# Kernel tuning notes

Hardware: AMD Instinct MI355X
Metric: run time of the kernel (lower is better)

The kernel has to match this reference:

```python
import jax, jax.numpy as jnp
import numpy as np

N_NODES = 50000
N_EDGES = 800000
IN_C, HID_C, OUT_C = 128, 256, 128


def _gcn_conv(x, src, dst, W, b, num_nodes):
    # PyG GCNConv: self-loops + symmetric normalization + linear + scatter-add
    deg = jax.ops.segment_sum(jnp.ones_like(src, x.dtype), dst, num_segments=num_nodes)
    dinv = jnp.where(deg > 0, jax.lax.rsqrt(deg), 0.0)
    norm = dinv[src] * dinv[dst]                      # [E']
    h = x @ W.T                                       # [N, C_out] transform first (C_out usually < C_in path cost)
    msg = h[src] * norm[:, None]                      # [E', C_out] gather + scale
    out = jax.ops.segment_sum(msg, dst, num_segments=num_nodes)  # scatter-add
    return out + b


def setup_inputs() -> dict:
    key = jax.random.key(0)
    k1, k2, k3, k4 = jax.random.split(key, 4)
    x = jax.random.normal(k1, (N_NODES, IN_C), dtype=jnp.float32)
    edge_index = jax.random.randint(k2, (2, N_EDGES), 0, N_NODES, dtype=jnp.int64)
    W1 = jax.random.normal(k3, (HID_C, IN_C), dtype=jnp.float32) * (1.0 / np.sqrt(IN_C))
    b1 = jnp.zeros((HID_C,), dtype=jnp.float32)
    W2 = jax.random.normal(k4, (OUT_C, HID_C), dtype=jnp.float32) * (1.0 / np.sqrt(HID_C))
    b2 = jnp.zeros((OUT_C,), dtype=jnp.float32)
    return {"x": x, "edge_index": edge_index, "W1": W1, "b1": b1,
            "W2": W2, "b2": b2, "num_nodes": N_NODES}


def reference(x, edge_index, W1, b1, W2, b2, num_nodes):
    # add self-loops once (shared by both layers)
    loop = jnp.arange(num_nodes, dtype=edge_index.dtype)
    src = jnp.concatenate([edge_index[0], loop])
    dst = jnp.concatenate([edge_index[1], loop])
    h = _gcn_conv(x, src, dst, W1, b1, num_nodes)
    h = jax.nn.relu(h)
    out = _gcn_conv(h, src, dst, W2, b2, num_nodes)
    return out
```

## Files before the change

kernel.cpp:

```cpp
#include <hip/hip_runtime.h>

#define N_NODES 50000
#define N_EDGES 800000
#define IN_C 128
#define HID_C 256
#define OUT_C 128
#define NBLK 196
#define NPART 8
#define PART_W 6250
#define KB2 32
#define CHUNK (N_EDGES / KB2)
#define HW_HIST 256
#define HW_W 16
#define SC_SCAT 256
#define SC_XC 1563

typedef __attribute__((ext_vector_type(8))) short short8v;
typedef __attribute__((ext_vector_type(4))) float f32x4;

static __device__ __forceinline__ unsigned short f2bf(float f) {
  unsigned int u = __float_as_uint(f);
  unsigned int r = (u + 0x7fffu + ((u >> 16) & 1u)) >> 16;
  return (unsigned short)r;
}
static __device__ __forceinline__ float bf2f(unsigned short h) {
  return __uint_as_float(((unsigned int)h) << 16);
}
static __device__ __forceinline__ unsigned int packBF2(float a, float b) {
  return (unsigned int)f2bf(a) | ((unsigned int)f2bf(b) << 16);
}

static __device__ __forceinline__ int detect64(const int* __restrict__ ei) {
  int nz = 0;
#pragma unroll
  for (int k = 0; k < 64; ++k) nz |= ei[2 * k + 1];
  return (nz == 0) ? 1 : 0;
}
static __device__ __forceinline__ int load_dst(const int* __restrict__ ei,
                                               int is64, int e) {
  return is64 ? (int)((const uint2*)ei)[N_EDGES + e].x : ei[N_EDGES + e];
}
static __device__ __forceinline__ int load_src(const int* __restrict__ ei,
                                               int is64, int e) {
  return is64 ? (int)((const uint2*)ei)[e].x : ei[e];
}

__global__ __launch_bounds__(1024) void hist_wconv_k(const int* __restrict__ ei,
                                                     int* __restrict__ H,
                                                     const float* __restrict__ W1,
                                                     unsigned int* __restrict__ w1bf,
                                                     const float* __restrict__ W2,
                                                     unsigned int* __restrict__ w2bf) {
  const int b = blockIdx.x;
  if (b < HW_HIST) {
    const int p = b & 7;
    const int c = b >> 3;
    __shared__ unsigned int hist[PART_W];
    __shared__ int s_is64;
    for (int i = threadIdx.x; i < PART_W; i += 1024) hist[i] = 0;
    if (threadIdx.x == 0) s_is64 = detect64(ei);
    __syncthreads();
    const int is64 = s_is64;
    const int s0 = c * CHUNK;
    for (int i = s0 + threadIdx.x; i < s0 + CHUNK; i += 1024) {
      const int d = load_dst(ei, is64, i);
      if (d / PART_W == p) atomicAdd(&hist[d - p * PART_W], 1u);
    }
    __syncthreads();
    int* Hrow = H + (p * KB2 + c) * PART_W;
    for (int i = threadIdx.x; i < PART_W; i += 1024) Hrow[i] = (int)hist[i];
  } else if (b < HW_HIST + HW_W) {
    const int i = (b - HW_HIST) * 1024 + threadIdx.x;
    const float2 f = *(const float2*)(W1 + (long)i * 2);
    w1bf[i] = packBF2(f.x, f.y);
  } else {
    const int i = (b - HW_HIST - HW_W) * 1024 + threadIdx.x;
    const float2 f = *(const float2*)(W2 + (long)i * 2);
    w2bf[i] = packBF2(f.x, f.y);
  }
}

__global__ __launch_bounds__(256) void bsum_k(const int* __restrict__ H,
                                              int* __restrict__ bsum) {
  const int i = blockIdx.x * 256 + threadIdx.x;
  int v = 0;
  if (i < N_NODES) {
    const int p = i / PART_W, bin = i % PART_W;
    const int* Hp = H + p * KB2 * PART_W + bin;
#pragma unroll
    for (int c = 0; c < KB2; ++c) v += Hp[c * PART_W];
  }
#pragma unroll
  for (int off = 32; off > 0; off >>= 1) v += __shfl_down(v, off, 64);
  __shared__ int ws[4];
  if ((threadIdx.x & 63) == 0) ws[threadIdx.x >> 6] = v;
  __syncthreads();
  if (threadIdx.x == 0) bsum[blockIdx.x] = ws[0] + ws[1] + ws[2] + ws[3];
}

__global__ __launch_bounds__(256) void bscan_k(const int* __restrict__ bsum,
                                               int* __restrict__ boff) {
  __shared__ int s[256];
  const int t = threadIdx.x;
  const int v = (t < NBLK) ? bsum[t] : 0;
  s[t] = v;
  __syncthreads();
  for (int off = 1; off < 256; off <<= 1) {
    const int tmp = (t >= off) ? s[t - off] : 0;
    __syncthreads();
    s[t] += tmp;
    __syncthreads();
  }
  if (t < NBLK) boff[t] = s[t] - v;
}

__global__ __launch_bounds__(256) void bfinal_k(int* __restrict__ H,
                                                const int* __restrict__ boff,
                                                int* __restrict__ rowstart,
                                                float* __restrict__ dinv) {
  __shared__ int s[256];
  const int t = threadIdx.x;
  const int i = blockIdx.x * 256 + t;
  int dtot = 0;
  int p = 0, bin = 0;
  if (i < N_NODES) {
    p = i / PART_W;
    bin = i % PART_W;
    int* Hp = H + p * KB2 * PART_W + bin;
#pragma unroll
    for (int c = 0; c < KB2; ++c) dtot += Hp[c * PART_W];
  }
  s[t] = dtot;
  __syncthreads();
  for (int off = 1; off < 256; off <<= 1) {
    const int tmp = (t >= off) ? s[t - off] : 0;
    __syncthreads();
    s[t] += tmp;
    __syncthreads();
  }
  const int run = boff[blockIdx.x] + s[t] - dtot;
  if (i < N_NODES) {
    rowstart[i] = run;
    dinv[i] = rsqrtf((float)dtot + 1.0f);
    int acc = run;
    int* Hp = H + p * KB2 * PART_W + bin;
#pragma unroll
    for (int c = 0; c < KB2; ++c) {
      const int cnt = Hp[c * PART_W];
      Hp[c * PART_W] = acc;
      acc += cnt;
    }
    if (i == N_NODES - 1) rowstart[N_NODES] = run + dtot;
  }
}

__global__ __launch_bounds__(1024) void scatter_xconv_k(
    const int* __restrict__ ei, const int* __restrict__ H,
    int* __restrict__ csr_src, const float* __restrict__ x,
    const float* __restrict__ dinv, unsigned int* __restrict__ xbf) {
  const int b = blockIdx.x;
  if (b < SC_SCAT) {
    const int p = b & 7;
    const int c = b >> 3;
    __shared__ unsigned int hist[PART_W];
    __shared__ int s_is64;
    for (int i = threadIdx.x; i < PART_W; i += 1024) hist[i] = 0;
    if (threadIdx.x == 0) s_is64 = detect64(ei);
    __syncthreads();
    const int is64 = s_is64;
    const int s0 = c * CHUNK;
    const int* Hrow = H + (p * KB2 + c) * PART_W;
    for (int i = s0 + threadIdx.x; i < s0 + CHUNK; i += 1024) {
      const int d = load_dst(ei, is64, i);
      if (d / PART_W == p) {
        const int ld = d - p * PART_W;
        const int lr = (int)atomicAdd(&hist[ld], 1u);
        csr_src[Hrow[ld] + lr] = load_src(ei, is64, i);
      }
    }
  } else {
    const int i = (b - SC_SCAT) * 1024 + threadIdx.x;
    if (i < N_NODES * IN_C / 4) {
      const int v = i >> 5;
      const float dv = dinv[v];
      const float4 f = *(const float4*)(x + (long)i * 4);
      uint2 u = {packBF2(dv * f.x, dv * f.y), packBF2(dv * f.z, dv * f.w)};
      *(uint2*)(xbf + (long)i * 2) = u;
    }
  }
}

__global__ __launch_bounds__(256) void gemm_fused_k(
    const unsigned int* __restrict__ X,
    const unsigned int* __restrict__ W1BF,
    const float* __restrict__ b1,
    const unsigned int* __restrict__ W2BF,
    const float* __restrict__ dinv,
    unsigned int* __restrict__ outBF) {
  constexpr int KP1 = 68;
  constexpr int HP = 132;
  __shared__ unsigned int xs[64 * KP1];
  __shared__ unsigned int h1s[64 * HP];

  const int tid = threadIdx.x;
  const int w = tid >> 6;
  const int l = tid & 63;
  const long nbase = (long)blockIdx.x * 64;
  const int kg = (l >> 4) * 8;
  const int lr = l & 15;
  const int mq0 = (l >> 4) * 4;

#pragma unroll
  for (int i = 0; i < 4; ++i) {
    const int idx = (tid + i * 256) * 4;
    const int row = idx >> 6, col = idx & 63;
    long gr = nbase + row;
    if (gr > N_NODES - 1) gr = N_NODES - 1;
    const uint4 v = *(const uint4*)(X + gr * 64 + col);
    *(uint4*)(xs + row * KP1 + col) = v;
  }
  __syncthreads();

  {
    const int m0w = w * 64;
    f32x4 acc[4][4];
#pragma unroll
    for (int nt = 0; nt < 4; ++nt)
#pragma unroll
      for (int mt = 0; mt < 4; ++mt) acc[nt][mt] = {0.0f, 0.0f, 0.0f, 0.0f};

#pragma unroll
    for (int ks = 0; ks < 4; ++ks) {
      const int ko = ks * 32 + kg;
      short8v wb[4];
#pragma unroll
      for (int mt = 0; mt < 4; ++mt)
        wb[mt] = *(const short8v*)(W1BF + (long)(m0w + mt * 16 + lr) * (IN_C / 2) +
                                   ko / 2);
#pragma unroll
      for (int nt = 0; nt < 4; ++nt) {
        const short8v xb = *(const short8v*)(xs + (nt * 16 + lr) * KP1 + ko / 2);
#pragma unroll
        for (int mt = 0; mt < 4; ++mt)
          acc[nt][mt] = __builtin_amdgcn_mfma_f32_16x16x32_bf16(wb[mt], xb,
                                                               acc[nt][mt], 0, 0, 0);
      }
    }

#pragma unroll
    for (int nt = 0; nt < 4; ++nt) {
      const int nl = nt * 16 + lr;
#pragma unroll
      for (int mt = 0; mt < 4; ++mt) {
        const int mq = m0w + mt * 16 + mq0;
        const float4 bv = *(const float4*)(b1 + mq);
        const float v0 = fmaxf(acc[nt][mt][0] + bv.x, 0.0f);
        const float v1 = fmaxf(acc[nt][mt][1] + bv.y, 0.0f);
        const float v2 = fmaxf(acc[nt][mt][2] + bv.z, 0.0f);
        const float v3 = fmaxf(acc[nt][mt][3] + bv.w, 0.0f);
        uint2 o = {packBF2(v0, v1), packBF2(v2, v3)};
        *(uint2*)(h1s + nl * HP + mq / 2) = o;
      }
    }
  }
  __syncthreads();

  {
    const int m0w = w * 32;
    f32x4 acc[4][2];
#pragma unroll
    for (int nt = 0; nt < 4; ++nt)
#pragma unroll
      for (int mt = 0; mt < 2; ++mt) acc[nt][mt] = {0.0f, 0.0f, 0.0f, 0.0f};

#pragma unroll
    for (int ks = 0; ks < 8; ++ks) {
      const int ko = ks * 32 + kg;
      short8v wb[2];
#pragma unroll
      for (int mt = 0; mt < 2; ++mt)
        wb[mt] = *(const short8v*)(W2BF + (long)(m0w + mt * 16 + lr) * (HID_C / 2) +
                                   ko / 2);
#pragma unroll
      for (int nt = 0; nt < 4; ++nt) {
        const short8v xb = *(const short8v*)(h1s + (nt * 16 + lr) * HP + ko / 2);
#pragma unroll
        for (int mt = 0; mt < 2; ++mt)
          acc[nt][mt] = __builtin_amdgcn_mfma_f32_16x16x32_bf16(wb[mt], xb,
                                                               acc[nt][mt], 0, 0, 0);
      }
    }

#pragma unroll
    for (int nt = 0; nt < 4; ++nt) {
      const long n = nbase + nt * 16 + lr;
      if (n < N_NODES) {
        const float dvn = dinv[n];
#pragma unroll
        for (int mt = 0; mt < 2; ++mt) {
          const int mq = m0w + mt * 16 + mq0;
          uint2 o = {packBF2(dvn * acc[nt][mt][0], dvn * acc[nt][mt][1]),
                     packBF2(dvn * acc[nt][mt][2], dvn * acc[nt][mt][3])};
          *(uint2*)(outBF + n * (OUT_C / 2) + mq / 2) = o;
        }
      }
    }
  }
}

template <int C, bool HAS_BIAS, bool OUT_BF>
__global__ __launch_bounds__(256) void gather_k(const int* __restrict__ rowstart,
                                                const int* __restrict__ csr_src,
                                                const float* __restrict__ dinv,
                                                const unsigned int* __restrict__ hbf,
                                                const float* __restrict__ bias,
                                                float* __restrict__ out,
                                                unsigned int* __restrict__ outBF) {
  const int v = (blockIdx.x * 256 + threadIdx.x) >> 6;
  if (v >= N_NODES) return;
  const int lane = threadIdx.x & 63;
  constexpr int CW = C / 2;
  const int rs = rowstart[v];
  const int re = rowstart[v + 1];
  const float dv = dinv[v];

  float a0 = 0.0f, a1 = 0.0f;

  int e = rs;
  for (; e + 15 < re; e += 16) {
    int s[16];
    unsigned int r[16];
#pragma unroll
    for (int j = 0; j < 16; ++j) s[j] = csr_src[e + j];
#pragma unroll
    for (int j = 0; j < 16; ++j) r[j] = hbf[(long)s[j] * CW + lane];
#pragma unroll
    for (int j = 0; j < 16; ++j) {
      a0 += bf2f((unsigned short)r[j]);
      a1 += bf2f((unsigned short)(r[j] >> 16));
    }
  }
  for (; e + 7 < re; e += 8) {
    int s[8];
    unsigned int r[8];
#pragma unroll
    for (int j = 0; j < 8; ++j) s[j] = csr_src[e + j];
#pragma unroll
    for (int j = 0; j < 8; ++j) r[j] = hbf[(long)s[j] * CW + lane];
#pragma unroll
    for (int j = 0; j < 8; ++j) {
      a0 += bf2f((unsigned short)r[j]);
      a1 += bf2f((unsigned short)(r[j] >> 16));
    }
  }
  for (; e + 3 < re; e += 4) {
    int s[4];
    unsigned int r[4];
#pragma unroll
    for (int j = 0; j < 4; ++j) s[j] = csr_src[e + j];
#pragma unroll
    for (int j = 0; j < 4; ++j) r[j] = hbf[(long)s[j] * CW + lane];
#pragma unroll
    for (int j = 0; j < 4; ++j) {
      a0 += bf2f((unsigned short)r[j]);
      a1 += bf2f((unsigned short)(r[j] >> 16));
    }
  }
  for (; e < re; ++e) {
    const unsigned int r0 = hbf[(long)csr_src[e] * CW + lane];
    a0 += bf2f((unsigned short)r0);
    a1 += bf2f((unsigned short)(r0 >> 16));
  }

  const unsigned int hv = hbf[(long)v * CW + lane];
  float o0 = dv * (a0 + bf2f((unsigned short)hv));
  float o1 = dv * (a1 + bf2f((unsigned short)(hv >> 16)));
  if (HAS_BIAS) {
    const float2 bv = *(const float2*)(bias + lane * 2);
    o0 += bv.x;
    o1 += bv.y;
  }
  if (OUT_BF) {
    outBF[(long)v * CW + lane] = packBF2(o0, o1);
  } else {
    const float2 o = {o0, o1};
    *(float2*)(out + (long)v * CW * 2 + lane * 2) = o;
  }
}

extern "C" void kernel_launch(void* const* d_in, const int* in_sizes, int n_in,
                              void* d_out, int out_size, void* d_ws, size_t ws_size,
                              hipStream_t stream) {
  (void)in_sizes; (void)n_in; (void)out_size; (void)ws_size;

  const float* x  = (const float*)d_in[0];
  const int*   ei = (const int*)d_in[1];
  const float* W1 = (const float*)d_in[2];
  const float* b1 = (const float*)d_in[3];
  const float* W2 = (const float*)d_in[4];
  const float* b2 = (const float*)d_in[5];
  float* out = (float*)d_out;

  char* ws = (char*)d_ws;
  int*   csr_src  = (int*)(ws + 3200000);
  int*   H        = (int*)(ws + 6400000);
  int*   rowstart = (int*)(ws + 12800000);
  float* dinv     = (float*)(ws + 13000512);
  int*   bsum     = (int*)(ws + 13200512);
  int*   boff     = (int*)(ws + 13201536);
  unsigned int* w1bf   = (unsigned int*)(ws + 13300000);
  unsigned int* w2bf   = (unsigned int*)(ws + 13400000);
  unsigned int* aggxbf = (unsigned int*)(ws + 14000000);
  unsigned int* h2bf   = (unsigned int*)(ws + 27000000);
  unsigned int* xbf    = (unsigned int*)(ws + 91200000);

  const int GB = (N_NODES + 3) / 4;

  hist_wconv_k<<<HW_HIST + 2 * HW_W, 1024, 0, stream>>>(ei, H, W1, w1bf, W2,
                                                        w2bf);
  bsum_k<<<NBLK, 256, 0, stream>>>(H, bsum);
  bscan_k<<<1, 256, 0, stream>>>(bsum, boff);
  bfinal_k<<<NBLK, 256, 0, stream>>>(H, boff, rowstart, dinv);
  scatter_xconv_k<<<SC_SCAT + SC_XC, 1024, 0, stream>>>(ei, H, csr_src, x,
                                                        dinv, xbf);

  gather_k<IN_C, false, true><<<GB, 256, 0, stream>>>(
      rowstart, csr_src, dinv, xbf, nullptr, nullptr, aggxbf);

  gemm_fused_k<<<(N_NODES + 63) / 64, 256, 0, stream>>>(aggxbf, w1bf, b1, w2bf,
                                                        dinv, h2bf);

  gather_k<OUT_C, true, false><<<GB, 256, 0, stream>>>(
      rowstart, csr_src, dinv, h2bf, b2, out, nullptr);
}
```

Before: 149.3 us.

## Fuse first-layer neighbor gather into the fused GEMM kernel

Each GEMM block now gathers and normalizes its 64 node rows directly from the bf16 features into shared memory, instead of reading a precomputed aggregated buffer. This removes one kernel launch and the global write and read of the intermediate aggregated features. The gather phase now runs with far fewer concurrent waves, each walking 16 rows sequentially, so there may be less memory-latency hiding. The gather loop is factored into a shared helper used by both the fused kernel and the final output gather.

```diff
diff --git a/kernel.cpp b/kernel.cpp
--- a/kernel.cpp
+++ b/kernel.cpp
@@ -45,6 +45,58 @@
   return is64 ? (int)((const uint2*)ei)[e].x : ei[e];
 }
 
+template <int CW>
+static __device__ __forceinline__ void gather_row(const int* __restrict__ csr_src,
+                                                  int rs, int re,
+                                                  const unsigned int* __restrict__ hbf,
+                                                  int lane, float& a0, float& a1) {
+  int e = rs;
+  for (; e + 15 < re; e += 16) {
+    int s[16];
+    unsigned int r[16];
+#pragma unroll
+    for (int j = 0; j < 16; ++j) s[j] = csr_src[e + j];
+#pragma unroll
+    for (int j = 0; j < 16; ++j) r[j] = hbf[(long)s[j] * CW + lane];
+#pragma unroll
+    for (int j = 0; j < 16; ++j) {
+      a0 += bf2f((unsigned short)r[j]);
+      a1 += bf2f((unsigned short)(r[j] >> 16));
+    }
+  }
+  for (; e + 7 < re; e += 8) {
+    int s[8];
+    unsigned int r[8];
+#pragma unroll
+    for (int j = 0; j < 8; ++j) s[j] = csr_src[e + j];
+#pragma unroll
+    for (int j = 0; j < 8; ++j) r[j] = hbf[(long)s[j] * CW + lane];
+#pragma unroll
+    for (int j = 0; j < 8; ++j) {
+      a0 += bf2f((unsigned short)r[j]);
+      a1 += bf2f((unsigned short)(r[j] >> 16));
+    }
+  }
+  for (; e + 3 < re; e += 4) {
+    int s[4];
+    unsigned int r[4];
+#pragma unroll
+    for (int j = 0; j < 4; ++j) s[j] = csr_src[e + j];
+#pragma unroll
+    for (int j = 0; j < 4; ++j) r[j] = hbf[(long)s[j] * CW + lane];
+#pragma unroll
+    for (int j = 0; j < 4; ++j) {
+      a0 += bf2f((unsigned short)r[j]);
+      a1 += bf2f((unsigned short)(r[j] >> 16));
+    }
+  }
+  for (; e < re; ++e) {
+    const unsigned int r0 = hbf[(long)csr_src[e] * CW + lane];
+    a0 += bf2f((unsigned short)r0);
+    a1 += bf2f((unsigned short)(r0 >> 16));
+  }
+}
+
 __global__ __launch_bounds__(1024) void hist_wconv_k(const int* __restrict__ ei,
                                                      int* __restrict__ H,
                                                      const float* __restrict__ W1,
@@ -190,13 +242,11 @@
   }
 }
 
-__global__ __launch_bounds__(256) void gemm_fused_k(
-    const unsigned int* __restrict__ X,
-    const unsigned int* __restrict__ W1BF,
-    const float* __restrict__ b1,
-    const unsigned int* __restrict__ W2BF,
-    const float* __restrict__ dinv,
-    unsigned int* __restrict__ outBF) {
+__global__ __launch_bounds__(256) void gather_gemm_fused_k(
+    const int* __restrict__ rowstart, const int* __restrict__ csr_src,
+    const float* __restrict__ dinv, const unsigned int* __restrict__ xbf,
+    const unsigned int* __restrict__ W1BF, const float* __restrict__ b1,
+    const unsigned int* __restrict__ W2BF, unsigned int* __restrict__ outBF) {
   constexpr int KP1 = 68;
   constexpr int HP = 132;
   __shared__ unsigned int xs[64 * KP1];
@@ -210,14 +260,22 @@
   const int lr = l & 15;
   const int mq0 = (l >> 4) * 4;
 
-#pragma unroll
-  for (int i = 0; i < 4; ++i) {
-    const int idx = (tid + i * 256) * 4;
-    const int row = idx >> 6, col = idx & 63;
-    long gr = nbase + row;
-    if (gr > N_NODES - 1) gr = N_NODES - 1;
-    const uint4 v = *(const uint4*)(X + gr * 64 + col);
-    *(uint4*)(xs + row * KP1 + col) = v;
+  for (int nn = 0; nn < 16; ++nn) {
+    const int row = w * 16 + nn;
+    const long v = nbase + row;
+    if (v < N_NODES) {
+      const int rs = rowstart[v];
+      const int re = rowstart[v + 1];
+      const float dv = dinv[v];
+      float a0 = 0.0f, a1 = 0.0f;
+      gather_row<64>(csr_src, rs, re, xbf, l, a0, a1);
+      const unsigned int hv = xbf[v * 64 + l];
+      const float o0 = dv * (a0 + bf2f((unsigned short)hv));
+      const float o1 = dv * (a1 + bf2f((unsigned short)(hv >> 16)));
+      xs[row * KP1 + l] = packBF2(o0, o1);
+    } else {
+      xs[row * KP1 + l] = 0u;
+    }
   }
   __syncthreads();
 
@@ -308,84 +366,30 @@
   }
 }
 
-template <int C, bool HAS_BIAS, bool OUT_BF>
-__global__ __launch_bounds__(256) void gather_k(const int* __restrict__ rowstart,
-                                                const int* __restrict__ csr_src,
-                                                const float* __restrict__ dinv,
-                                                const unsigned int* __restrict__ hbf,
-                                                const float* __restrict__ bias,
-                                                float* __restrict__ out,
-                                                unsigned int* __restrict__ outBF) {
+__global__ __launch_bounds__(256) void gather_out_k(const int* __restrict__ rowstart,
+                                                    const int* __restrict__ csr_src,
+                                                    const float* __restrict__ dinv,
+                                                    const unsigned int* __restrict__ hbf,
+                                                    const float* __restrict__ bias,
+                                                    float* __restrict__ out) {
   const int v = (blockIdx.x * 256 + threadIdx.x) >> 6;
   if (v >= N_NODES) return;
   const int lane = threadIdx.x & 63;
-  constexpr int CW = C / 2;
   const int rs = rowstart[v];
   const int re = rowstart[v + 1];
   const float dv = dinv[v];
 
   float a0 = 0.0f, a1 = 0.0f;
-
-  int e = rs;
-  for (; e + 15 < re; e += 16) {
-    int s[16];
-    unsigned int r[16];
-#pragma unroll
-    for (int j = 0; j < 16; ++j) s[j] = csr_src[e + j];
-#pragma unroll
-    for (int j = 0; j < 16; ++j) r[j] = hbf[(long)s[j] * CW + lane];
-#pragma unroll
-    for (int j = 0; j < 16; ++j) {
-      a0 += bf2f((unsigned short)r[j]);
-      a1 += bf2f((unsigned short)(r[j] >> 16));
-    }
-  }
-  for (; e + 7 < re; e += 8) {
-    int s[8];
-    unsigned int r[8];
-#pragma unroll
-    for (int j = 0; j < 8; ++j) s[j] = csr_src[e + j];
-#pragma unroll
-    for (int j = 0; j < 8; ++j) r[j] = hbf[(long)s[j] * CW + lane];
-#pragma unroll
-    for (int j = 0; j < 8; ++j) {
-      a0 += bf2f((unsigned short)r[j]);
-      a1 += bf2f((unsigned short)(r[j] >> 16));
-    }
-  }
-  for (; e + 3 < re; e += 4) {
-    int s[4];
-    unsigned int r[4];
-#pragma unroll
-    for (int j = 0; j < 4; ++j) s[j] = csr_src[e + j];
-#pragma unroll
-    for (int j = 0; j < 4; ++j) r[j] = hbf[(long)s[j] * CW + lane];
-#pragma unroll
-    for (int j = 0; j < 4; ++j) {
-      a0 += bf2f((unsigned short)r[j]);
-      a1 += bf2f((unsigned short)(r[j] >> 16));
-    }
-  }
-  for (; e < re; ++e) {
-    const unsigned int r0 = hbf[(long)csr_src[e] * CW + lane];
-    a0 += bf2f((unsigned short)r0);
-    a1 += bf2f((unsigned short)(r0 >> 16));
-  }
-
-  const unsigned int hv = hbf[(long)v * CW + lane];
+  gather_row<64>(csr_src, rs, re, hbf, lane, a0, a1);
+
+  const unsigned int hv = hbf[(long)v * 64 + lane];
   float o0 = dv * (a0 + bf2f((unsigned short)hv));
   float o1 = dv * (a1 + bf2f((unsigned short)(hv >> 16)));
-  if (HAS_BIAS) {
-    const float2 bv = *(const float2*)(bias + lane * 2);
-    o0 += bv.x;
-    o1 += bv.y;
-  }
-  if (OUT_BF) {
-    outBF[(long)v * CW + lane] = packBF2(o0, o1);
-  } else {
-    const float2 o = {o0, o1};
-    *(float2*)(out + (long)v * CW * 2 + lane * 2) = o;
-  }
+  const float2 bv = *(const float2*)(bias + lane * 2);
+  o0 += bv.x;
+  o1 += bv.y;
+  const float2 o = {o0, o1};
+  *(float2*)(out + (long)v * 128 + lane * 2) = o;
 }
 
 extern "C" void kernel_launch(void* const* d_in, const int* in_sizes, int n_in,
@@ -408,11 +412,10 @@
   float* dinv     = (float*)(ws + 13000512);
   int*   bsum     = (int*)(ws + 13200512);
   int*   boff     = (int*)(ws + 13201536);
-  unsigned int* w1bf   = (unsigned int*)(ws + 13300000);
-  unsigned int* w2bf   = (unsigned int*)(ws + 13400000);
-  unsigned int* aggxbf = (unsigned int*)(ws + 14000000);
-  unsigned int* h2bf   = (unsigned int*)(ws + 27000000);
-  unsigned int* xbf    = (unsigned int*)(ws + 91200000);
+  unsigned int* w1bf = (unsigned int*)(ws + 13300000);
+  unsigned int* w2bf = (unsigned int*)(ws + 13400000);
+  unsigned int* h2bf = (unsigned int*)(ws + 27000000);
+  unsigned int* xbf  = (unsigned int*)(ws + 91200000);
 
   const int GB = (N_NODES + 3) / 4;
 
@@ -424,12 +427,8 @@
   scatter_xconv_k<<<SC_SCAT + SC_XC, 1024, 0, stream>>>(ei, H, csr_src, x,
                                                         dinv, xbf);
 
-  gather_k<IN_C, false, true><<<GB, 256, 0, stream>>>(
-      rowstart, csr_src, dinv, xbf, nullptr, nullptr, aggxbf);
-
-  gemm_fused_k<<<(N_NODES + 63) / 64, 256, 0, stream>>>(aggxbf, w1bf, b1, w2bf,
-                                                        dinv, h2bf);
-
-  gather_k<OUT_C, true, false><<<GB, 256, 0, stream>>>(
-      rowstart, csr_src, dinv, h2bf, b2, out, nullptr);
-}
+  gather_gemm_fused_k<<<(N_NODES + 63) / 64, 256, 0, stream>>>(
+      rowstart, csr_src, dinv, xbf, w1bf, b1, w2bf, h2bf);
+
+  gather_out_k<<<GB, 256, 0, stream>>>(rowstart, csr_src, dinv, h2bf, b2, out);
+}
```

New measurement: 198.4 us. 32.9% more time.
